# Kernel tuning notes

Hardware: AMD Instinct MI355X
Metric: run time of the kernel (lower is better)

## Reference

```python
import jax, jax.numpy as jnp
import numpy as np

STRIDES = (8, 16, 32)
IMG = 640
REG_MAX = 16
TOPK = 10
ALPHA = 0.5
BETA = 6.0
EPS_IOU = 1e-16


def _make_anchors():
    # anchor centers for all pyramid levels, (N, 2) in pixel coords
    pts = []
    for s in STRIDES:
        h = w = IMG // s
        ys, xs = jnp.meshgrid(jnp.arange(h, dtype=jnp.float32),
                              jnp.arange(w, dtype=jnp.float32), indexing='ij')
        a = (jnp.stack([xs, ys], axis=-1).reshape(-1, 2) + 0.5) * s
        pts.append(a)
    return jnp.concatenate(pts, axis=0)  # (8400, 2)


def _iou_pairwise(pred, gt):
    # pred (B,N,4), gt (B,M,4) -> IoU (B,M,N)
    b1 = pred[:, None, :, :]   # (B,1,N,4)
    b2 = gt[:, :, None, :]     # (B,M,1,4)
    tl = jnp.maximum(b1[..., :2], b2[..., :2])
    br = jnp.minimum(b1[..., 2:], b2[..., 2:])
    wh = jnp.clip(br - tl, 0.0)
    inter = wh[..., 0] * wh[..., 1]
    a1 = (b1[..., 2] - b1[..., 0]) * (b1[..., 3] - b1[..., 1])
    a2 = (b2[..., 2] - b2[..., 0]) * (b2[..., 3] - b2[..., 1])
    return inter / (a1 + a2 - inter + EPS_IOU)


def _iou_1v1(b1, b2):
    # elementwise IoU, both (..., 4)
    tl = jnp.maximum(b1[..., :2], b2[..., :2])
    br = jnp.minimum(b1[..., 2:], b2[..., 2:])
    wh = jnp.clip(br - tl, 0.0)
    inter = wh[..., 0] * wh[..., 1]
    a1 = (b1[..., 2] - b1[..., 0]) * (b1[..., 3] - b1[..., 1])
    a2 = (b2[..., 2] - b2[..., 0]) * (b2[..., 3] - b2[..., 1])
    return inter / (a1 + a2 - inter + EPS_IOU)


def setup_inputs() -> dict:
    key = jax.random.key(0)
    ks = jax.random.split(key, 6)
    B, N, NC, M = 32, 8400, 80, 40
    pred_scores = jax.random.normal(ks[0], (B, N, NC), jnp.float32)
    pred_dist = jax.random.normal(ks[1], (B, N, 4 * REG_MAX), jnp.float32)
    gt_labels = jax.random.randint(ks[2], (B, M, 1), 0, NC, dtype=jnp.int32)
    cxy = jax.random.uniform(ks[3], (B, M, 2), jnp.float32) * 560.0 + 40.0
    wh = jax.random.uniform(ks[4], (B, M, 2), jnp.float32) * 120.0 + 20.0
    gt_bboxes = jnp.concatenate([jnp.clip(cxy - wh / 2, 0.0, float(IMG)),
                                 jnp.clip(cxy + wh / 2, 0.0, float(IMG))], axis=-1)
    dfl_weight = jax.random.normal(ks[5], (REG_MAX,), jnp.float32) * 0.05
    return {"pred_scores": pred_scores, "pred_dist": pred_dist,
            "gt_labels": gt_labels, "gt_bboxes": gt_bboxes,
            "dfl_weight": dfl_weight}


def reference(pred_scores, pred_dist, gt_labels, gt_bboxes, dfl_weight):
    B, N, NC = pred_scores.shape
    M = gt_bboxes.shape[1]
    anchors = _make_anchors()  # (N, 2)

    # DFL: softmax over reg bins, weighted sum with (random-init) conv weight
    prob = jax.nn.softmax(pred_dist.reshape(B, N, 4, REG_MAX), axis=-1)
    ltrb = prob @ dfl_weight                      # (B,N,4)
    pred_bboxes = jnp.concatenate([anchors - ltrb[..., :2],
                                   anchors + ltrb[..., 2:]], axis=-1)  # (B,N,4) xyxy

    # ---- task-aligned assigner (no-grad) ----
    sg = jax.lax.stop_gradient
    sig = jax.nn.sigmoid(sg(pred_scores))         # (B,N,NC)
    labels = gt_labels[..., 0].astype(jnp.int32)  # (B,M)
    sigT = jnp.swapaxes(sig, 1, 2)                # (B,NC,N)
    scores = jnp.take_along_axis(sigT, jnp.broadcast_to(labels[:, :, None], (B, M, N)), axis=1)  # (B,M,N)
    ious = jnp.clip(_iou_pairwise(sg(pred_bboxes), gt_bboxes), 0.0)      # (B,M,N)
    align = scores ** ALPHA * ious ** BETA        # (B,M,N)

    _, topk_idxs = jax.lax.top_k(align, TOPK)     # (B,M,TOPK) over anchors
    mask = jnp.zeros((B * M, N), dtype=align.dtype)
    mask = mask.at[jnp.arange(B * M)[:, None], topk_idxs.reshape(B * M, TOPK)].set(1.0)
    mask = mask.reshape(B, M, N)
    mask = mask * (align > 1e-9).astype(align.dtype)
    max_m = align.max(axis=1)                     # (B,N) best metric per anchor
    mask = mask * (align == max_m[:, None, :]).astype(align.dtype)

    fg_mask = mask.max(axis=1)                    # (B,N) in {0,1}
    tgt_idx = mask.argmax(axis=1)                 # (B,N) assigned gt index
    ts_sum = jnp.maximum(fg_mask.sum(), 1.0)

    # ---- classification targets (vectorized scatter) ----
    asg_labels = jnp.take_along_axis(labels, tgt_idx, axis=1)  # (B,N)
    target_scores = jax.nn.one_hot(asg_labels, NC, dtype=pred_scores.dtype) * (max_m * fg_mask)[..., None]

    x = pred_scores
    bce = jnp.maximum(x, 0.0) - x * target_scores + jnp.log1p(jnp.exp(-jnp.abs(x)))
    loss_cls = bce.sum() / ts_sum

    # ---- box IoU loss on positives (vectorized gather + mask) ----
    gt_asg = jnp.take_along_axis(gt_bboxes, tgt_idx[..., None], axis=1)  # (B,N,4)
    iou1 = _iou_1v1(pred_bboxes, gt_asg)          # (B,N)
    fg = fg_mask.sum()
    loss_box = jnp.where(fg > 0, ((1.0 - iou1) * fg_mask).sum() / fg, 0.0)

    return loss_cls + loss_box * 1.5
```

## Files before the change

kernel.cpp:

```cpp
#include <hip/hip_runtime.h>
#include <cstdint>
#include <cstddef>

#define BB 32
#define NN 8400
#define NCC 80
#define MM 40
#define RM 16
#define TOPKK 10
#define CAP 2048
#define SLOTP 41

__device__ __forceinline__ void anchor_xy(int n, float& ax, float& ay) {
    int s, x, y;
    if (n < 6400)      { s = 8;  y = n / 80;            x = n - y * 80; }
    else if (n < 8000) { int i = n - 6400; s = 16; y = i / 40; x = i - y * 40; }
    else               { int i = n - 8000; s = 32; y = i / 20; x = i - y * 20; }
    ax = ((float)x + 0.5f) * (float)s;
    ay = ((float)y + 0.5f) * (float)s;
}

__global__ __launch_bounds__(256) void k_dfl(const float* __restrict__ pd,
                                             const float* __restrict__ w,
                                             float* __restrict__ pbb) {
    int g = blockIdx.x * 256 + threadIdx.x;
    if (g >= BB * NN * 4) return;
    const float* p = pd + (size_t)g * RM;
    float x[RM];
    #pragma unroll
    for (int i = 0; i < 4; i++) {
        float4 v = *(const float4*)(p + i * 4);
        x[i*4+0] = v.x; x[i*4+1] = v.y; x[i*4+2] = v.z; x[i*4+3] = v.w;
    }
    float mx = x[0];
    #pragma unroll
    for (int i = 1; i < RM; i++) mx = fmaxf(mx, x[i]);
    float s = 0.f, d = 0.f;
    #pragma unroll
    for (int i = 0; i < RM; i++) {
        float e = __builtin_amdgcn_exp2f((x[i] - mx) * 1.44269504f);
        s += e; d += e * w[i];
    }
    float val = d * __builtin_amdgcn_rcpf(s);
    int bn = g >> 2, side = g & 3;
    int n = bn % NN;
    float ax, ay; anchor_xy(n, ax, ay);
    float coord = (side == 0) ? ax - val : (side == 1) ? ay - val
                : (side == 2) ? ax + val : ay + val;
    pbb[g] = coord;
}

__global__ __launch_bounds__(256) void k_align(const float* __restrict__ ps,
                                               const int*   __restrict__ gl,
                                               const float* __restrict__ gb,
                                               const float* __restrict__ pbb,
                                               float* __restrict__ maxm,
                                               int*   __restrict__ cnts,
                                               unsigned long long* __restrict__ lists,
                                               float* __restrict__ accum) {
    __shared__ float sc[128 * SLOTP];
    __shared__ float gtb[MM * 4];
    __shared__ int   glab[MM];
    __shared__ int   slotm[MM];
    __shared__ int   cmap[NCC];
    __shared__ float cm[256];
    __shared__ float redf[4];
    const int b  = blockIdx.y;
    const int n0 = blockIdx.x * 128;
    const int t  = threadIdx.x;

    if (t < MM * 4)              gtb[t] = gb[b * MM * 4 + t];
    if (t >= 192 && t < 192+MM)  glab[t - 192] = gl[b * MM + (t - 192)];
    if (t >= 64 && t < 64+NCC)   cmap[t - 64] = -1;
    __syncthreads();
    if (t == 0) {
        int ns = 0;
        for (int m = 0; m < MM; m++) {
            int c = glab[m];
            if (cmap[c] < 0) cmap[c] = ns++;
            slotm[m] = cmap[c];
        }
    }
    __syncthreads();

    float sp = 0.f;
    #pragma unroll
    for (int k = 0; k < 10; k++) {
        int f = t + k * 256;
        int row = f / 20, c4 = f - row * 20;
        int n = n0 + row;
        if (n < NN) {
            float4 v = *(const float4*)(ps + ((size_t)(b * NN + n)) * NCC + c4 * 4);
            float xs[4] = {v.x, v.y, v.z, v.w};
            #pragma unroll
            for (int j = 0; j < 4; j++) {
                float x = xs[j];
                float e = __builtin_amdgcn_exp2f(-1.44269504f * fabsf(x));
                float r = __builtin_amdgcn_rcpf(1.0f + e);
                sp += fmaxf(x, 0.f) + 0.69314718f * __builtin_amdgcn_logf(1.0f + e);
                int sl = cmap[c4 * 4 + j];
                if (sl >= 0) sc[row * SLOTP + sl] = (x >= 0.f) ? r : e * r;
            }
        }
    }
    __syncthreads();

    const int nloc = t & 127;
    const int n    = n0 + nloc;
    const int mb   = (t >> 7) * 20;
    const int lane = t & 63;
    const bool valid = (n < NN);
    float cmax = -INFINITY;
    float px1 = 0, py1 = 0, px2 = 0, py2 = 0, a1 = 0;
    if (valid) {
        float4 p4 = *(const float4*)(pbb + ((size_t)(b * NN + n)) * 4);
        px1 = p4.x; py1 = p4.y; px2 = p4.z; py2 = p4.w;
        a1 = (px2 - px1) * (py2 - py1);
    }
    #pragma unroll
    for (int j = 0; j < 20; j++) {
        int m = mb + j;
        float gx1 = gtb[m*4+0], gy1 = gtb[m*4+1], gx2 = gtb[m*4+2], gy2 = gtb[m*4+3];
        float a2 = (gx2 - gx1) * (gy2 - gy1);
        float iw = fmaxf(fminf(px2, gx2) - fmaxf(px1, gx1), 0.f);
        float ih = fmaxf(fminf(py2, gy2) - fmaxf(py1, gy1), 0.f);
        float inter = iw * ih;
        float iou = fmaxf(inter * __builtin_amdgcn_rcpf(a1 + a2 - inter + 1e-16f), 0.f);
        float al = 0.f;
        if (valid) {
            float sg = sc[nloc * SLOTP + slotm[m]];
            float i2 = iou * iou;
            al = __builtin_amdgcn_sqrtf(sg) * (i2 * i2 * i2);
        }
        cmax = fmaxf(cmax, al);
        bool pos = valid && (al > 1e-9f);
        unsigned long long msk = __ballot(pos);
        if (msk) {
            int leader = __ffsll((long long)msk) - 1;
            int basev = 0;
            if (lane == leader) basev = atomicAdd(&cnts[b * MM + m], __popcll(msk));
            basev = __shfl(basev, leader);
            if (pos) {
                int ofs = __popcll(msk & ((1ull << lane) - 1ull));
                int idx = basev + ofs;
                if (idx < CAP)
                    lists[((size_t)(b * MM + m)) * CAP + idx] =
                        ((unsigned long long)__float_as_uint(al) << 32) | (unsigned)n;
            }
        }
    }
    cm[t] = cmax;
    __syncthreads();
    if (t < 128 && valid) maxm[(size_t)b * NN + n] = fmaxf(cm[t], cm[t + 128]);

    #pragma unroll
    for (int off = 32; off > 0; off >>= 1) sp += __shfl_down(sp, off);
    if ((t & 63) == 0) redf[t >> 6] = sp;
    __syncthreads();
    if (t == 0) atomicAdd(accum, redf[0] + redf[1] + redf[2] + redf[3]);
}

__global__ __launch_bounds__(64) void k_topk(const unsigned long long* __restrict__ lists,
                                             const int*   __restrict__ cnts,
                                             const float* __restrict__ maxm,
                                             int* __restrict__ tgt) {
    __shared__ unsigned long long keys[CAP];
    const int bm = blockIdx.x, b = bm / MM, m = bm % MM, t = threadIdx.x;
    int cnt = min(cnts[bm], CAP);
    for (int i = t; i < cnt; i += 64) {
        unsigned long long L = lists[(size_t)bm * CAP + i];
        keys[i] = (L & 0xFFFFFFFF00000000ull) | (0xFFFFFFFFull - (L & 0xFFFFFFFFull));
    }
    __syncthreads();
    int kk = min(TOPKK, cnt);
    for (int p = 0; p < kk; p++) {
        unsigned long long best = 0ull;
        for (int i = t; i < cnt; i += 64) best = keys[i] > best ? keys[i] : best;
        #pragma unroll
        for (int off = 32; off > 0; off >>= 1) {
            unsigned long long o = __shfl_xor(best, off);
            best = o > best ? o : best;
        }
        for (int i = t; i < cnt; i += 64) if (keys[i] == best) keys[i] = 0ull;
        if (t == 0) {
            float v = __uint_as_float((unsigned)(best >> 32));
            int n = (int)(0xFFFFFFFFull - (best & 0xFFFFFFFFull));
            if (v == maxm[(size_t)b * NN + n]) atomicMin(&tgt[(size_t)b * NN + n], m);
        }
        __syncthreads();
    }
}

__global__ __launch_bounds__(256) void k_fg(const int*   __restrict__ tgt,
                                            const int*   __restrict__ gl,
                                            const float* __restrict__ gb,
                                            const float* __restrict__ ps,
                                            const float* __restrict__ pbb,
                                            const float* __restrict__ maxm,
                                            float* __restrict__ accum) {
    int i = blockIdx.x * 256 + threadIdx.x;
    int tg = tgt[i];
    if (tg >= MM) return;
    int b = i / NN;
    int lab = gl[b * MM + tg];
    float x = ps[(size_t)i * NCC + lab];
    float mm = maxm[i];
    float4 p = *(const float4*)(pbb + (size_t)i * 4);
    const float* g = gb + ((size_t)b * MM + tg) * 4;
    float a1 = (p.z - p.x) * (p.w - p.y);
    float a2 = (g[2] - g[0]) * (g[3] - g[1]);
    float iw = fmaxf(fminf(p.z, g[2]) - fmaxf(p.x, g[0]), 0.f);
    float ih = fmaxf(fminf(p.w, g[3]) - fmaxf(p.y, g[1]), 0.f);
    float inter = iw * ih;
    float iou = inter / (a1 + a2 - inter + 1e-16f);
    atomicAdd(&accum[1], x * mm);
    atomicAdd(&accum[2], 1.0f - iou);
    atomicAdd(&accum[3], 1.0f);
}

__global__ void k_final(const float* __restrict__ accum, float* __restrict__ out) {
    float S0 = accum[0], dot = accum[1], box = accum[2], fg = accum[3];
    float ts = fmaxf(fg, 1.0f);
    float cls = (S0 - dot) / ts;
    float lb = (fg > 0.f) ? box / fg : 0.f;
    out[0] = cls + 1.5f * lb;
}

extern "C" void kernel_launch(void* const* d_in, const int* in_sizes, int n_in,
                              void* d_out, int out_size, void* d_ws, size_t ws_size,
                              hipStream_t stream) {
    const float* ps = (const float*)d_in[0];
    const float* pd = (const float*)d_in[1];
    const int*   gl = (const int*)  d_in[2];
    const float* gb = (const float*)d_in[3];
    const float* w  = (const float*)d_in[4];

    char* ws = (char*)d_ws;
    constexpr size_t PBB_BYTES  = (size_t)BB * NN * 4 * sizeof(float);
    constexpr size_t MAXM_BYTES = (size_t)BB * NN * sizeof(float);
    constexpr size_t TGT_BYTES  = (size_t)BB * NN * sizeof(int);
    constexpr size_t CNT_BYTES  = 8192;
    constexpr size_t LIST_BYTES = (size_t)BB * MM * CAP * 8;

    float* accum = (float*)ws;
    float* pbb   = (float*)(ws + 256);
    float* maxm  = (float*)(ws + 256 + PBB_BYTES);
    int*   tgt   = (int*)  (ws + 256 + PBB_BYTES + MAXM_BYTES);
    int*   cnts  = (int*)  (ws + 256 + PBB_BYTES + MAXM_BYTES + TGT_BYTES);
    unsigned long long* lists =
        (unsigned long long*)(ws + 256 + PBB_BYTES + MAXM_BYTES + TGT_BYTES + CNT_BYTES);
    (void)LIST_BYTES;

    hipMemsetAsync(accum, 0, 8 * sizeof(float), stream);
    hipMemsetAsync(tgt, 0x7F, TGT_BYTES, stream);
    hipMemsetAsync(cnts, 0, CNT_BYTES, stream);

    k_dfl<<<(BB * NN * 4 + 255) / 256, 256, 0, stream>>>(pd, w, pbb);
    dim3 g3((NN + 127) / 128, BB);
    k_align<<<g3, 256, 0, stream>>>(ps, gl, gb, pbb, maxm, cnts, lists, accum);
    k_topk<<<BB * MM, 64, 0, stream>>>(lists, cnts, maxm, tgt);
    k_fg<<<BB * NN / 256, 256, 0, stream>>>(tgt, gl, gb, ps, pbb, maxm, accum);
    k_final<<<1, 1, 0, stream>>>(accum, (float*)d_out);
}
```

Baseline: 224.2 us.

## Fuse DFL decode into align kernel and reduce atomics in fg and topk

Folds the DFL softmax-expectation box decode into the alignment kernel, so decoded boxes stay in shared memory and one launch and the pbb re-read go away. The slot map is now built with a parallel atomicMin instead of a serial single-thread loop. Score loads are batched into registers before compute, with clamped indices replacing branches. k_fg replaces per-thread global atomics with wave and block reductions, and k_topk defers its atomics until after the selection loop, at the cost of more shared memory and register pressure in the fused kernel.

```diff
diff --git a/kernel.cpp b/kernel.cpp
--- a/kernel.cpp
+++ b/kernel.cpp
@@ -20,87 +20,92 @@
     ay = ((float)y + 0.5f) * (float)s;
 }
 
-__global__ __launch_bounds__(256) void k_dfl(const float* __restrict__ pd,
-                                             const float* __restrict__ w,
-                                             float* __restrict__ pbb) {
-    int g = blockIdx.x * 256 + threadIdx.x;
-    if (g >= BB * NN * 4) return;
-    const float* p = pd + (size_t)g * RM;
-    float x[RM];
-    #pragma unroll
-    for (int i = 0; i < 4; i++) {
-        float4 v = *(const float4*)(p + i * 4);
-        x[i*4+0] = v.x; x[i*4+1] = v.y; x[i*4+2] = v.z; x[i*4+3] = v.w;
-    }
-    float mx = x[0];
-    #pragma unroll
-    for (int i = 1; i < RM; i++) mx = fmaxf(mx, x[i]);
-    float s = 0.f, d = 0.f;
-    #pragma unroll
-    for (int i = 0; i < RM; i++) {
-        float e = __builtin_amdgcn_exp2f((x[i] - mx) * 1.44269504f);
-        s += e; d += e * w[i];
-    }
-    float val = d * __builtin_amdgcn_rcpf(s);
-    int bn = g >> 2, side = g & 3;
-    int n = bn % NN;
-    float ax, ay; anchor_xy(n, ax, ay);
-    float coord = (side == 0) ? ax - val : (side == 1) ? ay - val
-                : (side == 2) ? ax + val : ay + val;
-    pbb[g] = coord;
-}
-
-__global__ __launch_bounds__(256) void k_align(const float* __restrict__ ps,
-                                               const int*   __restrict__ gl,
-                                               const float* __restrict__ gb,
-                                               const float* __restrict__ pbb,
-                                               float* __restrict__ maxm,
-                                               int*   __restrict__ cnts,
-                                               unsigned long long* __restrict__ lists,
-                                               float* __restrict__ accum) {
-    __shared__ float sc[128 * SLOTP];
-    __shared__ float gtb[MM * 4];
-    __shared__ int   glab[MM];
-    __shared__ int   slotm[MM];
-    __shared__ int   cmap[NCC];
-    __shared__ float cm[256];
-    __shared__ float redf[4];
+__global__ __launch_bounds__(256) void k_main(const float* __restrict__ ps,
+                                              const float* __restrict__ pd,
+                                              const int*   __restrict__ gl,
+                                              const float* __restrict__ gb,
+                                              const float* __restrict__ w,
+                                              float* __restrict__ pbb,
+                                              float* __restrict__ maxm,
+                                              int*   __restrict__ cnts,
+                                              unsigned long long* __restrict__ lists,
+                                              float* __restrict__ accum) {
+    __shared__ float  sc[128 * SLOTP];
+    __shared__ float4 box[128];
+    __shared__ float  gtb[MM * 4];
+    __shared__ int    glab[MM];
+    __shared__ int    slotm[MM];
+    __shared__ int    cmap[NCC];
+    __shared__ float  cm[256];
+    __shared__ float  redf[4];
     const int b  = blockIdx.y;
     const int n0 = blockIdx.x * 128;
     const int t  = threadIdx.x;
 
     if (t < MM * 4)              gtb[t] = gb[b * MM * 4 + t];
     if (t >= 192 && t < 192+MM)  glab[t - 192] = gl[b * MM + (t - 192)];
-    if (t >= 64 && t < 64+NCC)   cmap[t - 64] = -1;
-    __syncthreads();
-    if (t == 0) {
-        int ns = 0;
-        for (int m = 0; m < MM; m++) {
-            int c = glab[m];
-            if (cmap[c] < 0) cmap[c] = ns++;
-            slotm[m] = cmap[c];
-        }
-    }
-    __syncthreads();
-
-    float sp = 0.f;
+    if (t >= 64 && t < 64+NCC)   cmap[t - 64] = 0x7FFFFFFF;
+    __syncthreads();
+    if (t < MM) atomicMin(&cmap[glab[t]], t);
+    __syncthreads();
+    if (t < MM) slotm[t] = cmap[glab[t]];
+
+    #pragma unroll
+    for (int h = 0; h < 2; h++) {
+        int f = t + h * 256;
+        int a = f >> 2, side = f & 3;
+        int nc = min(n0 + a, NN - 1);
+        const float* p = pd + (((size_t)(b * NN + nc)) * 4 + side) * RM;
+        float x[RM];
+        #pragma unroll
+        for (int i = 0; i < 4; i++) {
+            float4 v = *(const float4*)(p + i * 4);
+            x[i*4+0] = v.x; x[i*4+1] = v.y; x[i*4+2] = v.z; x[i*4+3] = v.w;
+        }
+        float mx = x[0];
+        #pragma unroll
+        for (int i = 1; i < RM; i++) mx = fmaxf(mx, x[i]);
+        float s = 0.f, d = 0.f;
+        #pragma unroll
+        for (int i = 0; i < RM; i++) {
+            float e = __builtin_amdgcn_exp2f((x[i] - mx) * 1.44269504f);
+            s += e; d += e * w[i];
+        }
+        ((float*)box)[f] = d * __builtin_amdgcn_rcpf(s);
+    }
+    __syncthreads();
+    if (t < 128) {
+        int n = n0 + t;
+        float ax, ay; anchor_xy(min(n, NN - 1), ax, ay);
+        float4 v = box[t];
+        float4 pb = make_float4(ax - v.x, ay - v.y, ax + v.z, ay + v.w);
+        box[t] = pb;
+        if (n < NN) *(float4*)(pbb + (size_t)(b * NN + n) * 4) = pb;
+    }
+
+    float4 vv[10];
     #pragma unroll
     for (int k = 0; k < 10; k++) {
         int f = t + k * 256;
         int row = f / 20, c4 = f - row * 20;
-        int n = n0 + row;
-        if (n < NN) {
-            float4 v = *(const float4*)(ps + ((size_t)(b * NN + n)) * NCC + c4 * 4);
-            float xs[4] = {v.x, v.y, v.z, v.w};
-            #pragma unroll
-            for (int j = 0; j < 4; j++) {
-                float x = xs[j];
-                float e = __builtin_amdgcn_exp2f(-1.44269504f * fabsf(x));
-                float r = __builtin_amdgcn_rcpf(1.0f + e);
-                sp += fmaxf(x, 0.f) + 0.69314718f * __builtin_amdgcn_logf(1.0f + e);
-                int sl = cmap[c4 * 4 + j];
-                if (sl >= 0) sc[row * SLOTP + sl] = (x >= 0.f) ? r : e * r;
-            }
+        int nc = min(n0 + row, NN - 1);
+        vv[k] = *(const float4*)(ps + ((size_t)(b * NN + nc)) * NCC + c4 * 4);
+    }
+    float sp = 0.f;
+    #pragma unroll
+    for (int k = 0; k < 10; k++) {
+        int f = t + k * 256;
+        int row = f / 20, c4 = f - row * 20;
+        float vmask = (n0 + row < NN) ? 1.f : 0.f;
+        float xs[4] = {vv[k].x, vv[k].y, vv[k].z, vv[k].w};
+        #pragma unroll
+        for (int j = 0; j < 4; j++) {
+            float x = xs[j];
+            float e = __builtin_amdgcn_exp2f(-1.44269504f * fabsf(x));
+            float r = __builtin_amdgcn_rcpf(1.0f + e);
+            sp += vmask * (fmaxf(x, 0.f) + 0.69314718f * __builtin_amdgcn_logf(1.0f + e));
+            int sl = cmap[c4 * 4 + j];
+            if (sl < MM) sc[row * SLOTP + sl] = (x >= 0.f) ? r : e * r;
         }
     }
     __syncthreads();
@@ -111,12 +116,9 @@
     const int lane = t & 63;
     const bool valid = (n < NN);
     float cmax = -INFINITY;
-    float px1 = 0, py1 = 0, px2 = 0, py2 = 0, a1 = 0;
-    if (valid) {
-        float4 p4 = *(const float4*)(pbb + ((size_t)(b * NN + n)) * 4);
-        px1 = p4.x; py1 = p4.y; px2 = p4.z; py2 = p4.w;
-        a1 = (px2 - px1) * (py2 - py1);
-    }
+    float4 p4 = box[nloc];
+    const float px1 = p4.x, py1 = p4.y, px2 = p4.z, py2 = p4.w;
+    const float a1 = (px2 - px1) * (py2 - py1);
     #pragma unroll
     for (int j = 0; j < 20; j++) {
         int m = mb + j;
@@ -165,14 +167,15 @@
                                              const float* __restrict__ maxm,
                                              int* __restrict__ tgt) {
     __shared__ unsigned long long keys[CAP];
+    __shared__ unsigned long long sel[TOPKK];
     const int bm = blockIdx.x, b = bm / MM, m = bm % MM, t = threadIdx.x;
     int cnt = min(cnts[bm], CAP);
+    int kk = min(TOPKK, cnt);
     for (int i = t; i < cnt; i += 64) {
         unsigned long long L = lists[(size_t)bm * CAP + i];
         keys[i] = (L & 0xFFFFFFFF00000000ull) | (0xFFFFFFFFull - (L & 0xFFFFFFFFull));
     }
     __syncthreads();
-    int kk = min(TOPKK, cnt);
     for (int p = 0; p < kk; p++) {
         unsigned long long best = 0ull;
         for (int i = t; i < cnt; i += 64) best = keys[i] > best ? keys[i] : best;
@@ -182,12 +185,14 @@
             best = o > best ? o : best;
         }
         for (int i = t; i < cnt; i += 64) if (keys[i] == best) keys[i] = 0ull;
-        if (t == 0) {
-            float v = __uint_as_float((unsigned)(best >> 32));
-            int n = (int)(0xFFFFFFFFull - (best & 0xFFFFFFFFull));
-            if (v == maxm[(size_t)b * NN + n]) atomicMin(&tgt[(size_t)b * NN + n], m);
-        }
+        if (t == 0) sel[p] = best;
         __syncthreads();
+    }
+    if (t < kk) {
+        unsigned long long bb = sel[t];
+        float v = __uint_as_float((unsigned)(bb >> 32));
+        int n = (int)(0xFFFFFFFFull - (bb & 0xFFFFFFFFull));
+        if (v == maxm[(size_t)b * NN + n]) atomicMin(&tgt[(size_t)b * NN + n], m);
     }
 }
 
@@ -199,23 +204,37 @@
                                             const float* __restrict__ maxm,
                                             float* __restrict__ accum) {
     int i = blockIdx.x * 256 + threadIdx.x;
+    int t = threadIdx.x;
+    float vdot = 0.f, vbox = 0.f, vfg = 0.f;
     int tg = tgt[i];
-    if (tg >= MM) return;
-    int b = i / NN;
-    int lab = gl[b * MM + tg];
-    float x = ps[(size_t)i * NCC + lab];
-    float mm = maxm[i];
-    float4 p = *(const float4*)(pbb + (size_t)i * 4);
-    const float* g = gb + ((size_t)b * MM + tg) * 4;
-    float a1 = (p.z - p.x) * (p.w - p.y);
-    float a2 = (g[2] - g[0]) * (g[3] - g[1]);
-    float iw = fmaxf(fminf(p.z, g[2]) - fmaxf(p.x, g[0]), 0.f);
-    float ih = fmaxf(fminf(p.w, g[3]) - fmaxf(p.y, g[1]), 0.f);
-    float inter = iw * ih;
-    float iou = inter / (a1 + a2 - inter + 1e-16f);
-    atomicAdd(&accum[1], x * mm);
-    atomicAdd(&accum[2], 1.0f - iou);
-    atomicAdd(&accum[3], 1.0f);
+    if (tg < MM) {
+        int b = i / NN;
+        int lab = gl[b * MM + tg];
+        float x = ps[(size_t)i * NCC + lab];
+        float mm = maxm[i];
+        float4 p = *(const float4*)(pbb + (size_t)i * 4);
+        const float* g = gb + ((size_t)b * MM + tg) * 4;
+        float a1 = (p.z - p.x) * (p.w - p.y);
+        float a2 = (g[2] - g[0]) * (g[3] - g[1]);
+        float iw = fmaxf(fminf(p.z, g[2]) - fmaxf(p.x, g[0]), 0.f);
+        float ih = fmaxf(fminf(p.w, g[3]) - fmaxf(p.y, g[1]), 0.f);
+        float inter = iw * ih;
+        float iou = inter / (a1 + a2 - inter + 1e-16f);
+        vdot = x * mm; vbox = 1.0f - iou; vfg = 1.0f;
+    }
+    #pragma unroll
+    for (int off = 32; off > 0; off >>= 1) {
+        vdot += __shfl_down(vdot, off);
+        vbox += __shfl_down(vbox, off);
+        vfg  += __shfl_down(vfg,  off);
+    }
+    __shared__ float r[3][4];
+    if ((t & 63) == 0) { int wv = t >> 6; r[0][wv] = vdot; r[1][wv] = vbox; r[2][wv] = vfg; }
+    __syncthreads();
+    if (t < 3) {
+        float s = r[t][0] + r[t][1] + r[t][2] + r[t][3];
+        if (s != 0.f) atomicAdd(&accum[1 + t], s);
+    }
 }
 
 __global__ void k_final(const float* __restrict__ accum, float* __restrict__ out) {
@@ -240,7 +259,6 @@
     constexpr size_t MAXM_BYTES = (size_t)BB * NN * sizeof(float);
     constexpr size_t TGT_BYTES  = (size_t)BB * NN * sizeof(int);
     constexpr size_t CNT_BYTES  = 8192;
-    constexpr size_t LIST_BYTES = (size_t)BB * MM * CAP * 8;
 
     float* accum = (float*)ws;
     float* pbb   = (float*)(ws + 256);
@@ -249,15 +267,13 @@
     int*   cnts  = (int*)  (ws + 256 + PBB_BYTES + MAXM_BYTES + TGT_BYTES);
     unsigned long long* lists =
         (unsigned long long*)(ws + 256 + PBB_BYTES + MAXM_BYTES + TGT_BYTES + CNT_BYTES);
-    (void)LIST_BYTES;
 
     hipMemsetAsync(accum, 0, 8 * sizeof(float), stream);
     hipMemsetAsync(tgt, 0x7F, TGT_BYTES, stream);
     hipMemsetAsync(cnts, 0, CNT_BYTES, stream);
 
-    k_dfl<<<(BB * NN * 4 + 255) / 256, 256, 0, stream>>>(pd, w, pbb);
     dim3 g3((NN + 127) / 128, BB);
-    k_align<<<g3, 256, 0, stream>>>(ps, gl, gb, pbb, maxm, cnts, lists, accum);
+    k_main<<<g3, 256, 0, stream>>>(ps, pd, gl, gb, w, pbb, maxm, cnts, lists, accum);
     k_topk<<<BB * MM, 64, 0, stream>>>(lists, cnts, maxm, tgt);
     k_fg<<<BB * NN / 256, 256, 0, stream>>>(tgt, gl, gb, ps, pbb, maxm, accum);
     k_final<<<1, 1, 0, stream>>>(accum, (float*)d_out);
```

New measurement: 198.7 us. 1.13x faster.
